# Optimization experiments

Hardware: AMD Instinct MI355X
Metric: run time of the kernel (lower is better)

The kernel has to match this reference:

```python
import jax, jax.numpy as jnp
import numpy as np

B, T, C, H, S = 4, 1024, 768, 12, 64  # batch, seq, emb_dim, n_heads, head_size
FF = 4 * C          # 3072, ff_hidden_size (required by SwiGLU input dim)
HID = int(8 * C / 3)  # 2048, SwiGLU hidden
EPS = 1e-6


def _rope_tables(seq_len, dim):
    # theta = 10000 ** (-2 * arange(0, dim, 2) / dim)  (note extra factor 2 vs standard RoPE)
    theta = 10000.0 ** (-2.0 * jnp.arange(0, dim, 2, dtype=jnp.float32) / dim)
    freqs = jnp.arange(seq_len, dtype=jnp.float32)[:, None] * theta  # [T, dim/2]
    cos = jnp.repeat(jnp.cos(freqs), 2, axis=-1)  # [T, dim]
    sin = jnp.repeat(jnp.sin(freqs), 2, axis=-1)
    return cos, sin


def _rope(x, cos, sin):
    # x: [..., T, S]; rotate pairs: even' = -odd, odd' = even
    rot = jnp.stack([-x[..., 1::2], x[..., 0::2]], axis=-1).reshape(x.shape)
    return x * cos + rot * sin


def _rmsnorm(x, gamma):
    # global scalar RMS over the whole tensor (faithful to torch.mean with no dim)
    return x / jnp.sqrt(EPS + jnp.mean(x * x)) * gamma


def _block(x, Wq, Wk, Wv, Wo, g1, g2, W1, b1, Ww, bw, Wg, bg, Wd, bd, W2, b2):
    Tlen = x.shape[1]
    cos, sin = _rope_tables(Tlen, S)
    # --- multi-head attention on rms1(x) ---
    h = _rmsnorm(x, g1)
    q = jnp.einsum('btc,hcs->bhts', h, Wq)
    k = jnp.einsum('btc,hcs->bhts', h, Wk)
    v = jnp.einsum('btc,hcs->bhts', h, Wv)
    rq = _rope(q, cos, sin)
    rk = _rope(k, cos, sin)
    scores = jnp.einsum('bhts,bhks->bhtk', rq, rk) * (C ** -0.5)  # scale by emb_dim, faithful
    causal = jnp.tril(jnp.ones((Tlen, Tlen), dtype=bool))
    scores = jnp.where(causal, scores, -jnp.inf)
    probs = jax.nn.softmax(scores, axis=-1)
    attn = jnp.einsum('bhtk,bhks->bhts', probs, v)
    attn = attn.transpose(0, 2, 1, 3).reshape(x.shape[0], Tlen, C)  # concat heads
    out = x + attn @ Wo
    # --- feed forward on rms2(out) ---
    h2 = _rmsnorm(out, g2)
    u = h2 @ W1 + b1                      # [B,T,FF]
    wx = u @ Ww + bw                      # [B,T,HID]
    vx = u @ Wg + bg
    ff = (wx * (vx * jax.nn.sigmoid(vx))) @ Wd + bd  # [B,T,FF]
    ff = ff @ W2 + b2                     # [B,T,C]
    return out + ff


def setup_inputs() -> dict:
    key = jax.random.key(0)
    ks = jax.random.split(key, 17)
    sd = 0.02
    return {
        'x':  jax.random.normal(ks[0], (B, T, C), jnp.float32),
        'Wq': jax.random.normal(ks[1], (H, C, S), jnp.float32) * sd,
        'Wk': jax.random.normal(ks[2], (H, C, S), jnp.float32) * sd,
        'Wv': jax.random.normal(ks[3], (H, C, S), jnp.float32) * sd,
        'Wo': jax.random.normal(ks[4], (C, C), jnp.float32) * sd,
        'g1': jnp.ones((C,), jnp.float32),
        'g2': jnp.ones((C,), jnp.float32),
        'W1': jax.random.normal(ks[5], (C, FF), jnp.float32) * sd,
        'b1': jnp.zeros((FF,), jnp.float32),
        'Ww': jax.random.normal(ks[6], (FF, HID), jnp.float32) * sd,
        'bw': jnp.zeros((HID,), jnp.float32),
        'Wg': jax.random.normal(ks[7], (FF, HID), jnp.float32) * sd,
        'bg': jnp.zeros((HID,), jnp.float32),
        'Wd': jax.random.normal(ks[8], (HID, FF), jnp.float32) * sd,
        'bd': jnp.zeros((FF,), jnp.float32),
        'W2': jax.random.normal(ks[9], (FF, C), jnp.float32) * sd,
        'b2': jnp.zeros((C,), jnp.float32),
    }


def reference(x, Wq, Wk, Wv, Wo, g1, g2, W1, b1, Ww, bw, Wg, bg, Wd, bd, W2, b2):
    return _block(x, Wq, Wk, Wv, Wo, g1, g2, W1, b1, Ww, bw, Wg, bg, Wd, bd, W2, b2)
```

## Files before the change

kernel.cpp:

```cpp
#include <hip/hip_runtime.h>
#include <math.h>

#define BB   4
#define TT   1024
#define CC   768
#define HH   12
#define SS   64
#define FFD  3072
#define HIDD 2048
#define NTOK (BB*TT)
#define EPSR 1e-6f

typedef __attribute__((ext_vector_type(8))) short bf16x8;
typedef __attribute__((ext_vector_type(4))) float f32x4;

__device__ __forceinline__ unsigned short f2bf(float f) {
    unsigned u = __float_as_uint(f);
    return (unsigned short)((u + 0x7FFFu + ((u >> 16) & 1u)) >> 16);
}
__device__ __forceinline__ float bfl(unsigned u) { return __uint_as_float(u << 16); }
__device__ __forceinline__ float bfh(unsigned u) { return __uint_as_float(u & 0xFFFF0000u); }
__device__ __forceinline__ unsigned pk2(float a, float b) {
    return (unsigned)f2bf(a) | ((unsigned)f2bf(b) << 16);
}

__device__ __forceinline__ void gload_lds16(const unsigned short* g, unsigned short* l) {
    __builtin_amdgcn_global_load_lds(
        (const __attribute__((address_space(1))) unsigned int*)g,
        (__attribute__((address_space(3))) unsigned int*)l, 16, 0, 0);
}

__global__ void k_sumsq_partial(const float* __restrict__ x, float* __restrict__ part, int n4) {
    __shared__ float sm[256];
    float s = 0.f;
    int stride = gridDim.x * blockDim.x;
    for (int i = blockIdx.x * blockDim.x + threadIdx.x; i < n4; i += stride) {
        float4 v = ((const float4*)x)[i];
        s += v.x*v.x + v.y*v.y + v.z*v.z + v.w*v.w;
    }
    sm[threadIdx.x] = s;
    __syncthreads();
    for (int off = 128; off > 0; off >>= 1) {
        if (threadIdx.x < off) sm[threadIdx.x] += sm[threadIdx.x + off];
        __syncthreads();
    }
    if (threadIdx.x == 0) part[blockIdx.x] = sm[0];
}

__global__ void k_sumsq_final(const float* __restrict__ part, float* __restrict__ outscale,
                              int npart, float invn) {
    __shared__ float sm[256];
    float s = 0.f;
    for (int i = threadIdx.x; i < npart; i += 256) s += part[i];
    sm[threadIdx.x] = s;
    __syncthreads();
    for (int off = 128; off > 0; off >>= 1) {
        if (threadIdx.x < off) sm[threadIdx.x] += sm[threadIdx.x + off];
        __syncthreads();
    }
    if (threadIdx.x == 0) outscale[0] = 1.0f / sqrtf(EPSR + sm[0] * invn);
}

__global__ void k_scale_gamma_b(const float* __restrict__ x, const float* __restrict__ g,
                                const float* __restrict__ scale, unsigned short* __restrict__ h,
                                int n8) {
    int i = blockIdx.x * blockDim.x + threadIdx.x;
    if (i >= n8) return;
    float sc = scale[0];
    float4 v0 = ((const float4*)x)[2*i];
    float4 v1 = ((const float4*)x)[2*i+1];
    int c = (i * 8) % CC;
    float4 g0 = *(const float4*)(g + c);
    float4 g1v = *(const float4*)(g + c + 4);
    uint4 r;
    r.x = pk2(v0.x*sc*g0.x,  v0.y*sc*g0.y);
    r.y = pk2(v0.z*sc*g0.z,  v0.w*sc*g0.w);
    r.z = pk2(v1.x*sc*g1v.x, v1.y*sc*g1v.y);
    r.w = pk2(v1.z*sc*g1v.z, v1.w*sc*g1v.w);
    ((uint4*)h)[i] = r;
}

__global__ void k_wT(const float* __restrict__ W, unsigned short* __restrict__ Wt,
                     int K, int N) {
    __shared__ float t[32][33];
    int k0 = blockIdx.x * 32, n0 = blockIdx.y * 32;
    int tx = threadIdx.x & 31, ty = threadIdx.x >> 5;
#pragma unroll
    for (int i = 0; i < 4; ++i)
        t[ty + i*8][tx] = W[(size_t)(k0 + ty + i*8) * N + n0 + tx];
    __syncthreads();
#pragma unroll
    for (int i = 0; i < 4; ++i)
        Wt[(size_t)(n0 + ty + i*8) * K + k0 + tx] = f2bf(t[tx][ty + i*8]);
}

__global__ void k_wqkvT(const float* __restrict__ Wq, const float* __restrict__ Wk,
                        const float* __restrict__ Wv, unsigned short* __restrict__ Wt) {
    __shared__ float t[32][33];
    int z = blockIdx.z, sel = z / HH, h = z % HH;
    const float* W = (sel == 0 ? Wq : (sel == 1 ? Wk : Wv)) + (size_t)h * CC * SS;
    int c0 = blockIdx.x * 32, s0 = blockIdx.y * 32;
    int tx = threadIdx.x & 31, ty = threadIdx.x >> 5;
#pragma unroll
    for (int i = 0; i < 4; ++i)
        t[ty + i*8][tx] = W[(size_t)(c0 + ty + i*8) * SS + s0 + tx];
    __syncthreads();
#pragma unroll
    for (int i = 0; i < 4; ++i)
        Wt[(size_t)(sel*CC + h*SS + s0 + ty + i*8) * CC + c0 + tx] = f2bf(t[tx][ty + i*8]);
}

__global__ void k_bcat(const float* __restrict__ bw, const float* __restrict__ bg,
                       float* __restrict__ bc) {
    int i = blockIdx.x * 256 + threadIdx.x;
    if (i >= 2*HIDD) return;
    bc[i] = (i < HIDD) ? bw[i] : bg[i - HIDD];
}

__global__ void k_rope_table(float* __restrict__ tab) {
    int i = blockIdx.x * blockDim.x + threadIdx.x;
    if (i >= TT * 32) return;
    int t = i >> 5, j = i & 31;
    float th = expf(-(float)j * 0.5756462732485115f);
    float ang = (float)t * th;
    tab[2*i]   = cosf(ang);
    tab[2*i+1] = sinf(ang);
}

__global__ void k_rope_apply_b(unsigned short* __restrict__ qkv, const float* __restrict__ tab) {
    int i = blockIdx.x * blockDim.x + threadIdx.x;
    if (i >= NTOK * HH * 32) return;
    int j  = i & 31;
    int h  = (i >> 5) % HH;
    int bt = i / (32 * HH);
    int t  = bt & (TT - 1);
    float cs = tab[(t*32 + j)*2];
    float sn = tab[(t*32 + j)*2 + 1];
    size_t base = (size_t)bt * (3*CC) + h * SS + 2*j;
    unsigned q = *(unsigned*)(qkv + base);
    float qe = bfl(q), qo = bfh(q);
    *(unsigned*)(qkv + base) = pk2(qe*cs - qo*sn, qo*cs + qe*sn);
    unsigned k = *(unsigned*)(qkv + base + CC);
    float ke = bfl(k), ko = bfh(k);
    *(unsigned*)(qkv + base + CC) = pk2(ke*cs - ko*sn, ko*cs + ke*sn);
}

__global__ void k_vT(const unsigned short* __restrict__ qkv, unsigned short* __restrict__ vtg) {
    int bh = blockIdx.x, ty = blockIdx.y;
    int b = bh / HH, h = bh % HH;
    int d = threadIdx.x & 63, tq = threadIdx.x >> 6;
    int t0 = ty * 128 + tq * 32;
    const unsigned short* src = qkv + (size_t)(b*TT + t0)*(3*CC) + 2*CC + h*SS + d;
    unsigned v[16];
#pragma unroll
    for (int e = 0; e < 16; ++e) {
        unsigned lo = src[(size_t)(2*e)*(3*CC)];
        unsigned hi = src[(size_t)(2*e+1)*(3*CC)];
        v[e] = (lo & 0xFFFFu) | (hi << 16);
    }
    uint4* dst = (uint4*)(vtg + ((size_t)bh*64 + d)*TT + t0);
#pragma unroll
    for (int q = 0; q < 4; ++q)
        dst[q] = make_uint4(v[q*4], v[q*4+1], v[q*4+2], v[q*4+3]);
}

template<bool BIAS, bool RES, bool OUTB>
__global__ __launch_bounds__(256) void k_gemm_bf16(
    const unsigned short* __restrict__ A, const unsigned short* __restrict__ Bt,
    const float* __restrict__ bias, const float* __restrict__ res,
    void* __restrict__ Cv, int M, int N, int K)
{
    __shared__ unsigned short As[2][128*32];
    __shared__ unsigned short Bs[2][128*32];
    const int tid  = threadIdx.x;
    const int w    = tid >> 6, lane = tid & 63;
    const int wr   = w >> 1,  wc   = w & 1;
    const int row0 = blockIdx.y * 128, col0 = blockIdx.x * 128;

    f32x4 acc[4][4];
#pragma unroll
    for (int m = 0; m < 4; ++m)
#pragma unroll
        for (int n = 0; n < 4; ++n) acc[m][n] = (f32x4){0.f, 0.f, 0.f, 0.f};

    const int lr4 = lane >> 2;
    const int scb = lane & 3;

    auto stage = [&](int t, int buf) {
#pragma unroll
        for (int i = 0; i < 2; ++i) {
            int lr = w * 32 + i * 16 + lr4;
            int cbs = scb ^ ((lr >> 1) & 3);
            const unsigned short* ga = A + (size_t)(row0 + lr) * K + t * 32 + cbs * 8;
            gload_lds16(ga, &As[buf][(w * 32 + i * 16) * 32]);
            const unsigned short* gb = Bt + (size_t)(col0 + lr) * K + t * 32 + cbs * 8;
            gload_lds16(gb, &Bs[buf][(w * 32 + i * 16) * 32]);
        }
    };

    const int nt = K / 32;
    stage(0, 0);
    int cur = 0;
    const int fr = lane & 15, fq = lane >> 4;
    for (int t = 0; t < nt; ++t) {
        __syncthreads();
        if (t + 1 < nt) stage(t + 1, cur ^ 1);
        bf16x8 af[4], bf[4];
#pragma unroll
        for (int m = 0; m < 4; ++m) {
            int ra = wr * 64 + m * 16 + fr;
            af[m] = *(const bf16x8*)&As[cur][ra * 32 + (fq ^ ((ra >> 1) & 3)) * 8];
            int rb = wc * 64 + m * 16 + fr;
            bf[m] = *(const bf16x8*)&Bs[cur][rb * 32 + (fq ^ ((rb >> 1) & 3)) * 8];
        }
#pragma unroll
        for (int m = 0; m < 4; ++m)
#pragma unroll
            for (int n = 0; n < 4; ++n)
                acc[m][n] = __builtin_amdgcn_mfma_f32_16x16x32_bf16(af[m], bf[n], acc[m][n], 0, 0, 0);
        cur ^= 1;
    }

#pragma unroll
    for (int m = 0; m < 4; ++m) {
#pragma unroll
        for (int n = 0; n < 4; ++n) {
            int col = col0 + wc * 64 + n * 16 + fr;
            float bv = BIAS ? bias[col] : 0.f;
#pragma unroll
            for (int j = 0; j < 4; ++j) {
                int row = row0 + wr * 64 + m * 16 + fq * 4 + j;
                size_t off = (size_t)row * N + col;
                float v = acc[m][n][j] + bv;
                if (RES) v += res[off];
                if (OUTB) ((unsigned short*)Cv)[off] = f2bf(v);
                else      ((float*)Cv)[off] = v;
            }
        }
    }
}

#define GSTEP(s_, DOSTAGE, GATE)                                                  \
    {                                                                             \
        const int st_ = (s_) & 3;                                                 \
        const unsigned short* pa_ = &ringA[st_][0];                               \
        const unsigned short* pb_ = &ringB[st_][0];                               \
        bf16x8 af[4], bv[4];                                                      \
        _Pragma("unroll")                                                         \
        for (int m = 0; m < 4; ++m) {                                             \
            int ra = wm*128 + m*16 + fr;                                          \
            af[m] = *(const bf16x8*)&pa_[ra*32 + (fq ^ ((ra>>1)&3))*8];           \
        }                                                                         \
        _Pragma("unroll")                                                         \
        for (int n = 0; n < 4; ++n) {                                             \
            int rb = wn*64 + n*16 + fr;                                           \
            bv[n] = *(const bf16x8*)&pb_[rb*32 + (fq ^ ((rb>>1)&3))*8];           \
        }                                                                         \
        if (DOSTAGE) stageA((s_) + 3);                                            \
        __builtin_amdgcn_sched_barrier(0);                                        \
        __builtin_amdgcn_s_barrier();                                             \
        asm volatile("s_waitcnt lgkmcnt(0)" ::: "memory");                        \
        __builtin_amdgcn_sched_barrier(0);                                        \
        __builtin_amdgcn_s_setprio(1);                                            \
        _Pragma("unroll")                                                         \
        for (int m = 0; m < 4; ++m)                                               \
            _Pragma("unroll")                                                     \
            for (int n = 0; n < 4; ++n)                                           \
                acc[m][n] = __builtin_amdgcn_mfma_f32_16x16x32_bf16(              \
                    af[m], bv[n], acc[m][n], 0, 0, 0);                            \
        __builtin_amdgcn_s_setprio(0);                                            \
        __builtin_amdgcn_sched_barrier(0);                                        \
        __builtin_amdgcn_s_barrier();                                             \
        _Pragma("unroll")                                                         \
        for (int m = 0; m < 4; ++m) {                                             \
            int ra = wm*128 + (m+4)*16 + fr;                                      \
            af[m] = *(const bf16x8*)&pa_[ra*32 + (fq ^ ((ra>>1)&3))*8];           \
        }                                                                         \
        if (DOSTAGE) stageB((s_) + 3);                                            \
        __builtin_amdgcn_sched_barrier(0);                                        \
        __builtin_amdgcn_s_barrier();                                             \
        asm volatile("s_waitcnt lgkmcnt(0)" ::: "memory");                        \
        __builtin_amdgcn_sched_barrier(0);                                        \
        __builtin_amdgcn_s_setprio(1);                                            \
        _Pragma("unroll")                                                         \
        for (int m = 0; m < 4; ++m)                                               \
            _Pragma("unroll")                                                     \
            for (int n = 0; n < 4; ++n)                                           \
                acc[m+4][n] = __builtin_amdgcn_mfma_f32_16x16x32_bf16(            \
                    af[m], bv[n], acc[m+4][n], 0, 0, 0);                          \
        __builtin_amdgcn_s_setprio(0);                                            \
        asm volatile("s_waitcnt " GATE ::: "memory");                             \
        __builtin_amdgcn_sched_barrier(0);                                        \
        __builtin_amdgcn_s_barrier();                                             \
    }

template<bool BIAS>
__global__ __launch_bounds__(512, 2) void k_gemm256(
    const unsigned short* __restrict__ A, const unsigned short* __restrict__ Bt,
    const float* __restrict__ bias, unsigned short* __restrict__ C,
    int M, int N, int K)
{
    __shared__ __align__(16) unsigned short ringA[4][256*32];
    __shared__ __align__(16) unsigned short ringB[4][256*32];
    const int tid = threadIdx.x;
    const int w = tid >> 6, lane = tid & 63;
    const int wm = w >> 2, wn = w & 3;
    const int fr = lane & 15, fq = lane >> 4;

    const int nwg = gridDim.x * gridDim.y;
    const int bid = blockIdx.y * gridDim.x + blockIdx.x;
    const int cpx = nwg >> 3;
    const int sbid = (bid & 7) * cpx + (bid >> 3);
    const int row0 = (sbid / gridDim.x) * 256;
    const int col0 = (sbid % gridDim.x) * 256;

    f32x4 acc[8][4];
#pragma unroll
    for (int m = 0; m < 8; ++m)
#pragma unroll
        for (int n = 0; n < 4; ++n) acc[m][n] = (f32x4){0.f, 0.f, 0.f, 0.f};

    auto stageA = [&](int t) {
        const int st = t & 3;
        const int kb = t * 32;
#pragma unroll
        for (int q = 0; q < 2; ++q) {
            int c = q * 512 + tid;
            int r = c >> 2;
            int part = (c & 3) ^ ((r >> 1) & 3);
            gload_lds16(A + (size_t)(row0 + r) * K + kb + part * 8,
                        &ringA[st][(q*512 + w*64) * 8]);
        }
    };
    auto stageB = [&](int t) {
        const int st = t & 3;
        const int kb = t * 32;
#pragma unroll
        for (int q = 0; q < 2; ++q) {
            int c = q * 512 + tid;
            int r = c >> 2;
            int part = (c & 3) ^ ((r >> 1) & 3);
            gload_lds16(Bt + (size_t)(col0 + r) * K + kb + part * 8,
                        &ringB[st][(q*512 + w*64) * 8]);
        }
    };

    const int S = K >> 5;
    stageA(0); stageB(0); stageA(1); stageB(1); stageA(2); stageB(2);
    asm volatile("s_waitcnt vmcnt(8)" ::: "memory");
    __builtin_amdgcn_s_barrier();
    int s = 0;
    for (; s < S - 3; ++s) GSTEP(s, true, "vmcnt(8)");
    GSTEP(s, false, "vmcnt(4)"); ++s;
    GSTEP(s, false, "vmcnt(0)"); ++s;
    GSTEP(s, false, "vmcnt(0)");

#pragma unroll
    for (int m = 0; m < 8; ++m) {
#pragma unroll
        for (int n = 0; n < 4; ++n) {
            int col = col0 + wn*64 + n*16 + fr;
            float bvb = BIAS ? bias[col] : 0.f;
#pragma unroll
            for (int j = 0; j < 4; ++j) {
                int row = row0 + wm*128 + m*16 + fq*4 + j;
                C[(size_t)row * N + col] = f2bf(acc[m][n][j] + bvb);
            }
        }
    }
}

__global__ __launch_bounds__(256) void k_attn_mfma(
    const unsigned short* __restrict__ qkv, const unsigned short* __restrict__ vtg,
    unsigned short* __restrict__ attn)
{
    __shared__ __align__(16) unsigned short Ks[2][64*64];
    __shared__ __align__(16) unsigned short Vs[2][64*64];
    __shared__ __align__(16) unsigned short Ps[4][16*72];
    const int tid = threadIdx.x;
    const int w = tid >> 6, lane = tid & 63;
    const int fr = lane & 15, fq = lane >> 4;
    const int bh = blockIdx.x, b = bh / HH, h = bh % HH;
    const int qb = blockIdx.y * 64;
    const int nkt = qb / 64 + 1;
    const float scale = 0.03608439182435161f;

    bf16x8 qf[2];
    {
        const unsigned short* qp = qkv + (size_t)(b*TT + qb + w*16 + fr)*(3*CC) + h*SS + fq*8;
        qf[0] = *(const bf16x8*)qp;
        qf[1] = *(const bf16x8*)(qp + 32);
    }

    auto stage = [&](int kt, int buf) {
        const unsigned short* kbase = qkv + (size_t)(b*TT + kt*64)*(3*CC) + CC + h*SS;
        const unsigned short* vbase = vtg + ((size_t)bh*64)*TT + kt*64;
#pragma unroll
        for (int p = 0; p < 2; ++p) {
            int s = p*256 + tid;
            int row = s >> 3;
            int blk = (s & 7) ^ (row & 7);
            gload_lds16(kbase + (size_t)row*(3*CC) + blk*8, &Ks[buf][(p*256 + w*64)*8]);
            gload_lds16(vbase + (size_t)row*TT + blk*8,     &Vs[buf][(p*256 + w*64)*8]);
        }
    };

    float m[4] = {-INFINITY, -INFINITY, -INFINITY, -INFINITY};
    float l[4] = {0.f, 0.f, 0.f, 0.f};
    f32x4 oacc[4];
#pragma unroll
    for (int n = 0; n < 4; ++n) oacc[n] = (f32x4){0.f, 0.f, 0.f, 0.f};

    stage(0, 0);
    int cur = 0;
    for (int kt = 0; kt < nkt; ++kt) {
        __syncthreads();
        if (kt + 1 < nkt) stage(kt + 1, cur ^ 1);

        f32x4 sacc[4];
#pragma unroll
        for (int n = 0; n < 4; ++n) sacc[n] = (f32x4){0.f, 0.f, 0.f, 0.f};
#pragma unroll
        for (int ks = 0; ks < 2; ++ks) {
#pragma unroll
            for (int n = 0; n < 4; ++n) {
                int row = n*16 + fr;
                bf16x8 kf = *(const bf16x8*)&Ks[cur][row*64 + ((ks*4 + fq) ^ (row & 7))*8];
                sacc[n] = __builtin_amdgcn_mfma_f32_16x16x32_bf16(qf[ks], kf, sacc[n], 0, 0, 0);
            }
        }

        float sv[4][4];
        const bool lastt = (kt == nkt - 1);
        const int qloc = w*16 + fq*4;
#pragma unroll
        for (int n = 0; n < 4; ++n) {
            int kloc = n*16 + fr;
#pragma unroll
            for (int j = 0; j < 4; ++j) {
                float vv = sacc[n][j] * scale;
                if (lastt && kloc > qloc + j) vv = -INFINITY;
                sv[j][n] = vv;
            }
        }
        float mx[4], ls[4];
#pragma unroll
        for (int j = 0; j < 4; ++j)
            mx[j] = fmaxf(fmaxf(sv[j][0], sv[j][1]), fmaxf(sv[j][2], sv[j][3]));
#pragma unroll
        for (int d = 1; d < 16; d <<= 1)
#pragma unroll
            for (int j = 0; j < 4; ++j) mx[j] = fmaxf(mx[j], __shfl_xor(mx[j], d));
        float corr[4];
#pragma unroll
        for (int j = 0; j < 4; ++j) {
            float nm = fmaxf(m[j], mx[j]);
            corr[j] = __expf(m[j] - nm);
            m[j] = nm;
        }
#pragma unroll
        for (int j = 0; j < 4; ++j) {
            float s0 = 0.f;
#pragma unroll
            for (int n = 0; n < 4; ++n) {
                float p = __expf(sv[j][n] - m[j]);
                sv[j][n] = p;
                s0 += p;
            }
            ls[j] = s0;
        }
#pragma unroll
        for (int d = 1; d < 16; d <<= 1)
#pragma unroll
            for (int j = 0; j < 4; ++j) ls[j] += __shfl_xor(ls[j], d);
#pragma unroll
        for (int j = 0; j < 4; ++j) l[j] = l[j]*corr[j] + ls[j];
#pragma unroll
        for (int n = 0; n < 4; ++n)
#pragma unroll
            for (int j = 0; j < 4; ++j) oacc[n][j] *= corr[j];

#pragma unroll
        for (int j = 0; j < 4; ++j)
#pragma unroll
            for (int n = 0; n < 4; ++n)
                Ps[w][(fq*4 + j)*72 + n*16 + fr] = f2bf(sv[j][n]);

#pragma unroll
        for (int ks = 0; ks < 2; ++ks) {
            bf16x8 pf = *(const bf16x8*)&Ps[w][fr*72 + ks*32 + fq*8];
#pragma unroll
            for (int n = 0; n < 4; ++n) {
                int row = n*16 + fr;
                bf16x8 vf = *(const bf16x8*)&Vs[cur][row*64 + ((ks*4 + fq) ^ (row & 7))*8];
                oacc[n] = __builtin_amdgcn_mfma_f32_16x16x32_bf16(pf, vf, oacc[n], 0, 0, 0);
            }
        }
        cur ^= 1;
    }

    float inv[4];
#pragma unroll
    for (int j = 0; j < 4; ++j) inv[j] = 1.0f / l[j];
#pragma unroll
    for (int n = 0; n < 4; ++n)
#pragma unroll
        for (int j = 0; j < 4; ++j) {
            size_t off = (size_t)(b*TT + qb + w*16 + fq*4 + j)*CC + h*SS + n*16 + fr;
            attn[off] = f2bf(oacc[n][j] * inv[j]);
        }
}

__global__ void k_swiglu_uv(const unsigned short* __restrict__ uv,
                            unsigned short* __restrict__ sw, int n8) {
    int i = blockIdx.x * blockDim.x + threadIdx.x;
    if (i >= n8) return;
    int r = i >> 8;
    int c8 = (i & 255) * 8;
    uint4 wv = *(const uint4*)(uv + (size_t)r * (2*HIDD) + c8);
    uint4 vv = *(const uint4*)(uv + (size_t)r * (2*HIDD) + HIDD + c8);
    uint4 rr;
    float w0, w1, v0, v1;
    w0 = bfl(wv.x); w1 = bfh(wv.x); v0 = bfl(vv.x); v1 = bfh(vv.x);
    rr.x = pk2(w0*v0/(1.f+__expf(-v0)), w1*v1/(1.f+__expf(-v1)));
    w0 = bfl(wv.y); w1 = bfh(wv.y); v0 = bfl(vv.y); v1 = bfh(vv.y);
    rr.y = pk2(w0*v0/(1.f+__expf(-v0)), w1*v1/(1.f+__expf(-v1)));
    w0 = bfl(wv.z); w1 = bfh(wv.z); v0 = bfl(vv.z); v1 = bfh(vv.z);
    rr.z = pk2(w0*v0/(1.f+__expf(-v0)), w1*v1/(1.f+__expf(-v1)));
    w0 = bfl(wv.w); w1 = bfh(wv.w); v0 = bfl(vv.w); v1 = bfh(vv.w);
    rr.w = pk2(w0*v0/(1.f+__expf(-v0)), w1*v1/(1.f+__expf(-v1)));
    *(uint4*)(sw + (size_t)r * HIDD + c8) = rr;
}

extern "C" void kernel_launch(void* const* d_in, const int* in_sizes, int n_in,
                              void* d_out, int out_size, void* d_ws, size_t ws_size,
                              hipStream_t stream)
{
    const float* x  = (const float*)d_in[0];
    const float* Wq = (const float*)d_in[1];
    const float* Wk = (const float*)d_in[2];
    const float* Wv = (const float*)d_in[3];
    const float* Wo = (const float*)d_in[4];
    const float* g1 = (const float*)d_in[5];
    const float* g2 = (const float*)d_in[6];
    const float* W1 = (const float*)d_in[7];
    const float* b1 = (const float*)d_in[8];
    const float* Ww = (const float*)d_in[9];
    const float* bw = (const float*)d_in[10];
    const float* Wg = (const float*)d_in[11];
    const float* bg = (const float*)d_in[12];
    const float* Wd = (const float*)d_in[13];
    const float* bd = (const float*)d_in[14];
    const float* W2 = (const float*)d_in[15];
    const float* b2 = (const float*)d_in[16];
    float* out = (float*)d_out;

    char* p = (char*)d_ws;
    auto alloc = [&](size_t bytes) { char* r = p; p += (bytes + 255) & ~(size_t)255; return r; };

    float*          scales = (float*)alloc(256);
    float*          part   = (float*)alloc(4096);
    float*          tab    = (float*)alloc((size_t)TT*32*2*4);
    float*          bcat   = (float*)alloc((size_t)2*HIDD*4);
    unsigned short* hb     = (unsigned short*)alloc((size_t)NTOK*CC*2);
    unsigned short* wqkvT  = (unsigned short*)alloc((size_t)3*CC*CC*2);
    unsigned short* qkvb   = (unsigned short*)alloc((size_t)NTOK*3*CC*2);
    unsigned short* vtg    = (unsigned short*)alloc((size_t)BB*HH*SS*TT*2);
    unsigned short* attnb  = (unsigned short*)alloc((size_t)NTOK*CC*2);
    unsigned short* WoT    = (unsigned short*)alloc((size_t)CC*CC*2);
    unsigned short* W1T    = (unsigned short*)alloc((size_t)FFD*CC*2);
    unsigned short* ub     = (unsigned short*)alloc((size_t)NTOK*FFD*2);
    unsigned short* WcatT  = (unsigned short*)alloc((size_t)2*HIDD*FFD*2);
    unsigned short* uvcat  = (unsigned short*)alloc((size_t)NTOK*2*HIDD*2);
    unsigned short* swb    = (unsigned short*)alloc((size_t)NTOK*HIDD*2);
    unsigned short* WdT    = (unsigned short*)alloc((size_t)FFD*HIDD*2);
    unsigned short* W2T    = (unsigned short*)alloc((size_t)CC*FFD*2);

    const int n = NTOK * CC;

    k_wqkvT<<<dim3(CC/32, SS/32, 36), 256, 0, stream>>>(Wq, Wk, Wv, wqkvT);
    k_wT<<<dim3(CC/32,  CC/32),  256, 0, stream>>>(Wo, WoT, CC,  CC);
    k_wT<<<dim3(CC/32,  FFD/32), 256, 0, stream>>>(W1, W1T, CC,  FFD);
    k_wT<<<dim3(FFD/32, HIDD/32),256, 0, stream>>>(Ww, WcatT, FFD, HIDD);
    k_wT<<<dim3(FFD/32, HIDD/32),256, 0, stream>>>(Wg, WcatT + (size_t)HIDD*FFD, FFD, HIDD);
    k_wT<<<dim3(HIDD/32,FFD/32), 256, 0, stream>>>(Wd, WdT, HIDD,FFD);
    k_wT<<<dim3(FFD/32, CC/32),  256, 0, stream>>>(W2, W2T, FFD, CC);
    k_bcat<<<(2*HIDD)/256, 256, 0, stream>>>(bw, bg, bcat);
    k_rope_table<<<(TT*32)/256, 256, 0, stream>>>(tab);

    k_sumsq_partial<<<1024, 256, 0, stream>>>(x, part, n/4);
    k_sumsq_final<<<1, 256, 0, stream>>>(part, scales + 0, 1024, 1.0f/(float)n);
    k_scale_gamma_b<<<(n/8)/256, 256, 0, stream>>>(x, g1, scales + 0, hb, n/8);

    k_gemm256<false><<<dim3(3*CC/256, NTOK/256), 512, 0, stream>>>(
        hb, wqkvT, nullptr, qkvb, NTOK, 3*CC, CC);
    k_rope_apply_b<<<(NTOK*HH*32)/256, 256, 0, stream>>>(qkvb, tab);
    k_vT<<<dim3(BB*HH, TT/128), 256, 0, stream>>>(qkvb, vtg);

    k_attn_mfma<<<dim3(BB*HH, TT/64), 256, 0, stream>>>(qkvb, vtg, attnb);

    k_gemm_bf16<false,true,false><<<dim3(CC/128, NTOK/128), 256, 0, stream>>>(
        attnb, WoT, nullptr, x, out, NTOK, CC, CC);

    k_sumsq_partial<<<1024, 256, 0, stream>>>(out, part, n/4);
    k_sumsq_final<<<1, 256, 0, stream>>>(part, scales + 1, 1024, 1.0f/(float)n);
    k_scale_gamma_b<<<(n/8)/256, 256, 0, stream>>>(out, g2, scales + 1, hb, n/8);

    k_gemm256<true><<<dim3(FFD/256, NTOK/256), 512, 0, stream>>>(
        hb, W1T, b1, ub, NTOK, FFD, CC);
    k_gemm256<true><<<dim3(2*HIDD/256, NTOK/256), 512, 0, stream>>>(
        ub, WcatT, bcat, uvcat, NTOK, 2*HIDD, FFD);
    k_swiglu_uv<<<(NTOK*HIDD/8)/256, 256, 0, stream>>>(uvcat, swb, NTOK*HIDD/8);
    k_gemm256<true><<<dim3(FFD/256, NTOK/256), 512, 0, stream>>>(
        swb, WdT, bd, ub, NTOK, FFD, HIDD);
    k_gemm_bf16<true,true,false><<<dim3(CC/128, NTOK/128), 256, 0, stream>>>(
        ub, W2T, b2, out, out, NTOK, CC, FFD);
}
```

Measured before the change: 430.2 us.

## Double-buffer GEMM LDS fragments in registers and drop intra-step barriers

```diff
diff --git a/kernel.cpp b/kernel.cpp
--- a/kernel.cpp
+++ b/kernel.cpp
@@ -240,26 +240,17 @@
     }
 }
 
-#define GSTEP(s_, DOSTAGE, GATE)                                                  \
+#define PHASES(s_, CA, CB, NA, NB, DOSTAGE, DONEXT, GATE)                         \
     {                                                                             \
         const int st_ = (s_) & 3;                                                 \
-        const unsigned short* pa_ = &ringA[st_][0];                               \
-        const unsigned short* pb_ = &ringB[st_][0];                               \
-        bf16x8 af[4], bv[4];                                                      \
+        const int nx_ = ((s_) + 1) & 3;                                           \
+        bf16x8 afHi[4];                                                           \
         _Pragma("unroll")                                                         \
         for (int m = 0; m < 4; ++m) {                                             \
-            int ra = wm*128 + m*16 + fr;                                          \
-            af[m] = *(const bf16x8*)&pa_[ra*32 + (fq ^ ((ra>>1)&3))*8];           \
-        }                                                                         \
-        _Pragma("unroll")                                                         \
-        for (int n = 0; n < 4; ++n) {                                             \
-            int rb = wn*64 + n*16 + fr;                                           \
-            bv[n] = *(const bf16x8*)&pb_[rb*32 + (fq ^ ((rb>>1)&3))*8];           \
+            int ra = wm*128 + (m+4)*16 + fr;                                      \
+            afHi[m] = *(const bf16x8*)&ringA[st_][ra*32 + (fq ^ ((ra>>1)&3))*8];  \
         }                                                                         \
         if (DOSTAGE) stageA((s_) + 3);                                            \
-        __builtin_amdgcn_sched_barrier(0);                                        \
-        __builtin_amdgcn_s_barrier();                                             \
-        asm volatile("s_waitcnt lgkmcnt(0)" ::: "memory");                        \
         __builtin_amdgcn_sched_barrier(0);                                        \
         __builtin_amdgcn_s_setprio(1);                                            \
         _Pragma("unroll")                                                         \
@@ -267,19 +258,22 @@
             _Pragma("unroll")                                                     \
             for (int n = 0; n < 4; ++n)                                           \
                 acc[m][n] = __builtin_amdgcn_mfma_f32_16x16x32_bf16(              \
-                    af[m], bv[n], acc[m][n], 0, 0, 0);                            \
+                    CA[m], CB[n], acc[m][n], 0, 0, 0);                            \
         __builtin_amdgcn_s_setprio(0);                                            \
         __builtin_amdgcn_sched_barrier(0);                                        \
-        __builtin_amdgcn_s_barrier();                                             \
-        _Pragma("unroll")                                                         \
-        for (int m = 0; m < 4; ++m) {                                             \
-            int ra = wm*128 + (m+4)*16 + fr;                                      \
-            af[m] = *(const bf16x8*)&pa_[ra*32 + (fq ^ ((ra>>1)&3))*8];           \
+        if (DONEXT) {                                                             \
+            _Pragma("unroll")                                                     \
+            for (int m = 0; m < 4; ++m) {                                         \
+                int ra = wm*128 + m*16 + fr;                                      \
+                NA[m] = *(const bf16x8*)&ringA[nx_][ra*32 + (fq ^ ((ra>>1)&3))*8];\
+            }                                                                     \
+            _Pragma("unroll")                                                     \
+            for (int n = 0; n < 4; ++n) {                                         \
+                int rb = wn*64 + n*16 + fr;                                       \
+                NB[n] = *(const bf16x8*)&ringB[nx_][rb*32 + (fq ^ ((rb>>1)&3))*8];\
+            }                                                                     \
         }                                                                         \
         if (DOSTAGE) stageB((s_) + 3);                                            \
-        __builtin_amdgcn_sched_barrier(0);                                        \
-        __builtin_amdgcn_s_barrier();                                             \
-        asm volatile("s_waitcnt lgkmcnt(0)" ::: "memory");                        \
         __builtin_amdgcn_sched_barrier(0);                                        \
         __builtin_amdgcn_s_setprio(1);                                            \
         _Pragma("unroll")                                                         \
@@ -287,9 +281,9 @@
             _Pragma("unroll")                                                     \
             for (int n = 0; n < 4; ++n)                                           \
                 acc[m+4][n] = __builtin_amdgcn_mfma_f32_16x16x32_bf16(            \
-                    af[m], bv[n], acc[m+4][n], 0, 0, 0);                          \
+                    afHi[m], CB[n], acc[m+4][n], 0, 0, 0);                        \
         __builtin_amdgcn_s_setprio(0);                                            \
-        asm volatile("s_waitcnt " GATE ::: "memory");                             \
+        asm volatile("s_waitcnt " GATE);                                          \
         __builtin_amdgcn_sched_barrier(0);                                        \
         __builtin_amdgcn_s_barrier();                                             \
     }
@@ -347,13 +341,30 @@
 
     const int S = K >> 5;
     stageA(0); stageB(0); stageA(1); stageB(1); stageA(2); stageB(2);
-    asm volatile("s_waitcnt vmcnt(8)" ::: "memory");
+    asm volatile("s_waitcnt vmcnt(4)");
     __builtin_amdgcn_s_barrier();
+
+    bf16x8 afL0[4], bv0[4], afL1[4], bv1[4];
+#pragma unroll
+    for (int m = 0; m < 4; ++m) {
+        int ra = wm*128 + m*16 + fr;
+        afL0[m] = *(const bf16x8*)&ringA[0][ra*32 + (fq ^ ((ra>>1)&3))*8];
+    }
+#pragma unroll
+    for (int n = 0; n < 4; ++n) {
+        int rb = wn*64 + n*16 + fr;
+        bv0[n] = *(const bf16x8*)&ringB[0][rb*32 + (fq ^ ((rb>>1)&3))*8];
+    }
+
     int s = 0;
-    for (; s < S - 3; ++s) GSTEP(s, true, "vmcnt(8)");
-    GSTEP(s, false, "vmcnt(4)"); ++s;
-    GSTEP(s, false, "vmcnt(0)"); ++s;
-    GSTEP(s, false, "vmcnt(0)");
+    for (; s < S - 4; s += 2) {
+        PHASES(s,   afL0, bv0, afL1, bv1, true, true, "vmcnt(4)");
+        PHASES(s+1, afL1, bv1, afL0, bv0, true, true, "vmcnt(4)");
+    }
+    PHASES(S-4, afL0, bv0, afL1, bv1, true,  true,  "vmcnt(4)");
+    PHASES(S-3, afL1, bv1, afL0, bv0, false, true,  "vmcnt(0)");
+    PHASES(S-2, afL0, bv0, afL1, bv1, false, true,  "vmcnt(0)");
+    PHASES(S-1, afL1, bv1, afL0, bv0, false, false, "vmcnt(0)");
 
 #pragma unroll
     for (int m = 0; m < 8; ++m) {
```

Measured after the change: 441.5 us. +2.6%, slower.
